# Performance work log

Hardware: AMD Instinct MI355X
Metric: run time of the kernel (lower is better)

The kernel has to match this reference:

```python
import jax, jax.numpy as jnp
import numpy as np

UNITS = 4096                                # number of heap nodes (power of two)
DEPTH = (UNITS - 1).bit_length() + 1        # 13 heap steps (k = 0..12)
FEATURES = [2, 64, 64, 2]
BATCH = 256


def _build_heap_maps(nodes):
    """For each heap step k, precompute for every output node j the input
    (ancestor) node index it reads from, plus a validity mask. This encodes
    exactly the torch block loop: for level l, input nodes [floor(2^(l-1)), 2^l)
    broadcast (repeat_interleave by heap_factor) into output range
    [out_node0, out_node1), with blocks where out_node1 > nodes skipped."""
    depth = (nodes - 1).bit_length() + 1
    maps = []
    for k in range(depth):
        idx = np.zeros(nodes, np.int32)
        mask = np.zeros(nodes, np.bool_)
        for l in range(depth):
            in0 = 0 if l == 0 else 2 ** (l - 1)
            if in0 == 0:  # root block (node 0)
                hf = 1 if k == 0 else 2 ** (k - 1)      # ceil(2^(k-1))
                out0 = 0 if k == 0 else 2 ** (k - 1)    # floor(2^(k-1))
                out1 = out0 + hf
            else:
                hf = 2 ** k
                out0 = in0 * hf
                out1 = (2 ** l) * hf
            if out1 <= nodes:
                js = np.arange(out0, out1)
                idx[js] = in0 + (js - out0) // hf
                mask[js] = True
        maps.append((jnp.asarray(idx), jnp.asarray(mask)))
    return maps


MAPS = _build_heap_maps(UNITS)


def heap_linear(x, W, b, minheap):
    # x: [..., nodes, in_f]; W: [K, out_f, in_f]; b: [K, out_f]; K = DEPTH - minheap
    out = jnp.zeros(x.shape[:-1] + (W.shape[1],), jnp.float32)
    for i, k in enumerate(range(minheap, DEPTH)):
        idx, mask = MAPS[k]
        # apply linear_k to every node once, then gather parent -> children
        y = jnp.einsum('...ni,oi->...no', x, W[i]) + b[i]
        out = out + jnp.where(mask[:, None], y[..., idx, :], 0.0)
    return out


def setup_inputs() -> dict:
    key = jax.random.key(0)
    ks = jax.random.split(key, 7)
    f0, f1, f2, f3 = FEATURES

    def w(k, n, o, i):
        return jax.random.normal(k, (n, o, i), jnp.float32) / np.float32(np.sqrt(i))

    return {
        "x": jax.random.normal(ks[0], (BATCH, UNITS, f0), jnp.float32),
        "W1": w(ks[1], DEPTH - 1, f1, f0),   # minheap=1 -> 12 sublayers
        "b1": jax.random.normal(ks[2], (DEPTH - 1, f1), jnp.float32) * 0.01,
        "W2": w(ks[3], DEPTH, f2, f1),       # minheap=0 -> 13 sublayers
        "b2": jax.random.normal(ks[4], (DEPTH, f2), jnp.float32) * 0.01,
        "W3": w(ks[5], DEPTH, f3, f2),
        "b3": jax.random.normal(ks[6], (DEPTH, f3), jnp.float32) * 0.01,
    }


def reference(x, W1, b1, W2, b2, W3, b3):
    h = heap_linear(x, W1, b1, minheap=1)
    h = jax.nn.relu(h)
    h = heap_linear(h, W2, b2, minheap=0)
    h = jax.nn.relu(h)
    logits = heap_linear(h, W3, b3, minheap=0)
    return logits
```

## Files before the change

kernel.cpp:

```cpp
#include <hip/hip_runtime.h>

#define UNITS 4096
#define DEPTH 13
#define BATCH 256

typedef __attribute__((ext_vector_type(8))) short s16x8;
typedef __attribute__((ext_vector_type(4))) float f32x4;
typedef __attribute__((ext_vector_type(4))) int   i32x4;

__device__ __forceinline__ unsigned short f2bf(float f){
  unsigned u = __builtin_bit_cast(unsigned, f);
  u += 0x7FFFu + ((u >> 16) & 1u);
  return (unsigned short)(u >> 16);
}
__device__ __forceinline__ int levelof(int j){ return j ? (32 - __clz(j)) : 0; }

struct FragA { s16x8 v[2][2]; };
struct FragB { s16x8 v[2][4]; };

__device__ __forceinline__ void load_afrag(FragA& f, const unsigned short* __restrict__ Hq,
                                           int rowbase, int l15, int kg){
  #pragma unroll
  for (int kk = 0; kk < 2; ++kk)
    #pragma unroll
    for (int m = 0; m < 2; ++m)
      f.v[kk][m] = *(const s16x8*)(Hq + ((size_t)((kk*4 + kg)*256 + rowbase + m*16 + l15))*8);
}
__device__ __forceinline__ void load_bfrag(FragB& f, const unsigned short* __restrict__ Wf,
                                           int lane){
  #pragma unroll
  for (int kk = 0; kk < 2; ++kk)
    #pragma unroll
    for (int n = 0; n < 4; ++n)
      f.v[kk][n] = *(const s16x8*)(Wf + ((size_t)((kk*4 + n)*64 + lane))*8);
}
__device__ __forceinline__ void mstep(f32x4 acc[2][4], const FragA& A, const FragB& B){
  #pragma unroll
  for (int kk = 0; kk < 2; ++kk)
    #pragma unroll
    for (int m = 0; m < 2; ++m)
      #pragma unroll
      for (int n = 0; n < 4; ++n)
        acc[m][n] = __builtin_amdgcn_mfma_f32_16x16x32_bf16(A.v[kk][m], B.v[kk][n], acc[m][n], 0, 0, 0);
}
__device__ __forceinline__ void negA(FragA& A){
  const i32x4 sgn = {(int)0x80008000, (int)0x80008000, (int)0x80008000, (int)0x80008000};
  #pragma unroll
  for (int kk = 0; kk < 2; ++kk)
    #pragma unroll
    for (int m = 0; m < 2; ++m){
      i32x4 t = __builtin_bit_cast(i32x4, A.v[kk][m]);
      t ^= sgn;
      A.v[kk][m] = __builtin_bit_cast(s16x8, t);
    }
}

__device__ __forceinline__ float rowsum16(float s){
  int v, u;
  v = __builtin_bit_cast(int, s);
  u = __builtin_amdgcn_update_dpp(v, v, 0xB1, 0xF, 0xF, false);
  s += __builtin_bit_cast(float, u);
  v = __builtin_bit_cast(int, s);
  u = __builtin_amdgcn_update_dpp(v, v, 0x4E, 0xF, 0xF, false);
  s += __builtin_bit_cast(float, u);
  v = __builtin_bit_cast(int, s);
  u = __builtin_amdgcn_update_dpp(v, v, 0x141, 0xF, 0xF, false);
  s += __builtin_bit_cast(float, u);
  v = __builtin_bit_cast(int, s);
  u = __builtin_amdgcn_update_dpp(v, v, 0x140, 0xF, 0xF, false);
  s += __builtin_bit_cast(float, u);
  return s;
}

__device__ __forceinline__ void epilogue(const f32x4 acc[2][4], int p, int lp,
    const float cbv[4], const float* w3s,
    float* __restrict__ y3, int rowbase, int l15, int kg){
  int tmax = 11 - lp;
  for (int tt = 0; tt <= tmax; ++tt){
    float w30[4], w31[4];
    #pragma unroll
    for (int n = 0; n < 4; ++n){
      w30[n] = w3s[(tt*2 + 0)*64 + n*16 + l15];
      w31[n] = w3s[(tt*2 + 1)*64 + n*16 + l15];
    }
    int off = 4096 - (4096 >> tt);
    #pragma unroll
    for (int m = 0; m < 2; ++m)
      #pragma unroll
      for (int reg = 0; reg < 4; ++reg){
        float s0 = 0.f, s1 = 0.f;
        #pragma unroll
        for (int n = 0; n < 4; ++n){
          float hv = fmaxf(acc[m][n][reg] + cbv[n], 0.f);
          s0 = fmaf(w30[n], hv, s0);
          s1 = fmaf(w31[n], hv, s1);
        }
        s0 = rowsum16(s0);
        s1 = rowsum16(s1);
        if (l15 == 0){
          int b = rowbase + m*16 + kg*4 + reg;
          float2 v; v.x = s0; v.y = s1;
          *(float2*)(y3 + ((size_t)(off + p)*256 + b)*2) = v;
        }
      }
  }
}

__global__ __launch_bounds__(256) void k_prep(const float* __restrict__ W2,
    const float* __restrict__ W1, const float* __restrict__ W3,
    const float* __restrict__ b1, const float* __restrict__ b2, const float* __restrict__ b3,
    unsigned short* __restrict__ W2f, unsigned short* __restrict__ W1f,
    float* __restrict__ cb1, float* __restrict__ cb2, float* __restrict__ cb3,
    float* __restrict__ w3h20){
  int blk = blockIdx.x, t = threadIdx.x;
  if (blk < 26){
    int u = blk*256 + t;
    int lane = u & 63, c = (u >> 6) & 7, k = u >> 9;
    int n = c & 3, kk = c >> 2, l15 = lane & 15, kg = lane >> 4;
    s16x8 rr;
    #pragma unroll
    for (int e = 0; e < 8; ++e)
      rr[e] = (short)f2bf(W2[((size_t)(k*64 + n*16 + l15))*64 + kk*32 + kg*8 + e]);
    *(s16x8*)(W2f + (size_t)u*8) = rr;
  } else if (blk == 26){
    int n = t >> 6, lane = t & 63, l15 = lane & 15, kg = lane >> 4;
    int f = n*16 + l15;
    s16x8 r = {0,0,0,0,0,0,0,0};
    #pragma unroll
    for (int j = 0; j < 4; ++j){
      int m = kg*4 + j;
      if (m < DEPTH-1){
        r[2*j]   = (short)f2bf(W1[(m*64 + f)*2]);
        r[2*j+1] = (short)f2bf(W1[(m*64 + f)*2 + 1]);
      }
    }
    *(s16x8*)(W1f + (size_t)t*8) = r;
  } else {
    if (t < 64){
      float r = 0.f;
      cb1[t] = 0.f;
      for (int m = 1; m < DEPTH; ++m){ r += b1[(m-1)*64 + t]; cb1[m*64 + t] = r; }
      float r2 = 0.f;
      for (int m = 0; m < DEPTH; ++m){ r2 += b2[m*64 + t]; cb2[m*64 + t] = r2; }
    } else if (t < 66){
      int o = t - 64;
      float r = 0.f;
      for (int m = 0; m < DEPTH; ++m){ r += b3[m*2 + o]; cb3[m*2 + o] = r; }
    } else if (t >= 128 && t < 128 + DEPTH*2){
      int q = t - 128, tt = q >> 1, o = q & 1;
      float s = 0.f;
      for (int f = 0; f < 64; ++f)
        s = fmaf(W3[(tt*2 + o)*64 + f], fmaxf(b2[f], 0.f), s);
      w3h20[tt*2 + o] = s;
    }
  }
}

__global__ __launch_bounds__(256) void k_xpose(const float* __restrict__ x,
                                               float* __restrict__ xT){
  __shared__ float2 tile[64][65];
  int jb = (blockIdx.x & 63) * 64;
  int bb = (blockIdx.x >> 6) * 64;
  int t = threadIdx.x;
  #pragma unroll
  for (int i = 0; i < 16; ++i){
    int idx = i*256 + t;
    int jj = idx & 63, b = idx >> 6;
    tile[jj][b] = *(const float2*)(x + (((size_t)(bb + b))*UNITS + jb + jj)*2);
  }
  __syncthreads();
  #pragma unroll
  for (int i = 0; i < 16; ++i){
    int idx = i*256 + t;
    int b = idx & 63, jj = idx >> 6;
    *(float2*)(xT + (((size_t)(jb + jj))*BATCH + bb + b)*2) = tile[jj][b];
  }
}

__global__ __launch_bounds__(256) void k_GH(const float* __restrict__ xT,
    const unsigned short* __restrict__ W1f, const float* __restrict__ cb1,
    unsigned short* __restrict__ H){
  __shared__ unsigned short tile[BATCH*64];
  int p = blockIdx.x;
  int lvl = levelof(p);
  int t = threadIdx.x, wid = t >> 6, lane = t & 63, l15 = lane & 15, kg = lane >> 4;

  s16x8 af[4];
  #pragma unroll
  for (int m = 0; m < 4; ++m){
    int b = wid*64 + m*16 + l15;
    s16x8 r = {0,0,0,0,0,0,0,0};
    #pragma unroll
    for (int j = 0; j < 4; ++j){
      int mm = kg*4 + j;
      if (mm <= lvl){
        float2 xv = *(const float2*)(xT + ((size_t)(p >> mm)*BATCH + b)*2);
        r[2*j]   = (short)f2bf(xv.x);
        r[2*j+1] = (short)f2bf(xv.y);
      }
    }
    af[m] = r;
  }
  f32x4 acc[4][4];
  #pragma unroll
  for (int m = 0; m < 4; ++m)
    #pragma unroll
    for (int n = 0; n < 4; ++n) acc[m][n] = (f32x4){0.f,0.f,0.f,0.f};
  #pragma unroll
  for (int n = 0; n < 4; ++n){
    s16x8 bf = *(const s16x8*)(W1f + ((size_t)n*64 + lane)*8);
    #pragma unroll
    for (int m = 0; m < 4; ++m)
      acc[m][n] = __builtin_amdgcn_mfma_f32_16x16x32_bf16(af[m], bf, acc[m][n], 0, 0, 0);
  }
  int lvl1 = lvl + 1;
  float cbv[4];
  #pragma unroll
  for (int n = 0; n < 4; ++n) cbv[n] = cb1[lvl1*64 + n*16 + l15];
  #pragma unroll
  for (int m = 0; m < 4; ++m)
    #pragma unroll
    for (int n = 0; n < 4; ++n)
      #pragma unroll
      for (int i = 0; i < 4; ++i){
        int row = wid*64 + m*16 + kg*4 + i;
        int col = n*16 + l15;
        float v = fmaxf(acc[m][n][i] + cbv[n], 0.f);
        *(unsigned short*)((char*)tile + ((row*128 + col*2) ^ ((row & 7) << 4))) = f2bf(v);
      }
  __syncthreads();
  #pragma unroll
  for (int i = 0; i < 8; ++i){
    s16x8 v = *(const s16x8*)((const char*)tile + ((t*128 + i*16) ^ ((t & 7) << 4)));
    *(s16x8*)(H + (size_t)p*16384 + ((size_t)i*256 + t)*8) = v;
  }
}

#define CHB(slot, kk) if ((kk) <= L) load_bfrag(b##slot, W2f + (size_t)(kk)*4096, lane);
#define CHA(slot, ss) if ((ss)+2 <= L) load_afrag(a##slot, H + ((size_t)(q >> (ss)))*16384, rowbase, l15, kg);
#define CHM(as, bs, ss) if ((ss)+2 <= L) mstep(acc, a##as, b##bs);

__global__ __launch_bounds__(256) void k_F7(const unsigned short* __restrict__ H,
    const unsigned short* __restrict__ W2f, const float* __restrict__ cb2,
    const float* __restrict__ W3, float* __restrict__ y3){
  __shared__ float w3s[26*64];
  int bid = blockIdx.x;
  int sg  = bid >> 9;
  int r   = bid & 511;
  int q   = (r & 7)*64 + (r >> 3);
  int t = threadIdx.x, wid = t >> 6, lane = t & 63, l15 = lane & 15, kg = lane >> 4;
  int rowbase = sg*128 + wid*32;

  #pragma unroll
  for (int i = 0; i < 2; ++i){
    int idx = i*256 + t;
    if (idx < 416) ((float4*)w3s)[idx] = ((const float4*)W3)[idx];
  }
  __syncthreads();

  f32x4 acc[2][4];
  #pragma unroll
  for (int m = 0; m < 2; ++m)
    #pragma unroll
    for (int n = 0; n < 4; ++n) acc[m][n] = (f32x4){0.f,0.f,0.f,0.f};

  if (q == 0){
    FragA A; FragB B;
    for (int p = 0; p < 4; ++p){
      int lp = levelof(p);
      float cbv[4];
      #pragma unroll
      for (int n = 0; n < 4; ++n) cbv[n] = cb2[(lp+1)*64 + n*16 + l15];
      #pragma unroll
      for (int m = 0; m < 2; ++m)
        #pragma unroll
        for (int n = 0; n < 4; ++n) acc[m][n] = (f32x4){0.f,0.f,0.f,0.f};
      for (int k = 0; k <= lp; ++k){
        load_bfrag(B, W2f + (size_t)k*4096, lane);
        load_afrag(A, H + (size_t)(p >> k)*16384, rowbase, l15, kg);
        mstep(acc, A, B);
      }
      epilogue(acc, p, lp, cbv, w3s, y3, rowbase, l15, kg);
    }
    return;
  }

  const int L = levelof(q) + 2;
  float cbv[4];
  #pragma unroll
  for (int n = 0; n < 4; ++n) cbv[n] = cb2[(L+1)*64 + n*16 + l15];

  FragA a0, a1, a2; FragB b0, b1;

  CHB(0,2) CHB(1,3)
  CHA(0,0) CHA(1,1) CHA(2,2)
  CHM(0,0,0) CHB(0,4)  CHA(0,3)
  CHM(1,1,1) CHB(1,5)  CHA(1,4)
  CHM(2,0,2) CHB(0,6)  CHA(2,5)
  CHM(0,1,3) CHB(1,7)  CHA(0,6)
  CHM(1,0,4) CHB(0,8)  CHA(1,7)
  CHM(2,1,5) CHB(1,9)  CHA(2,8)
  CHM(0,0,6) CHB(0,10) CHA(0,9)
  CHM(1,1,7) CHB(1,11)
  load_afrag(a1, H + (size_t)(2*q)*16384, rowbase, l15, kg);
  CHM(2,0,8)
  load_bfrag(b0, W2f + 4096, lane);
  load_afrag(a2, H + (size_t)(4*q)*16384, rowbase, l15, kg);
  CHM(0,1,9)
  load_bfrag(b1, W2f, lane);
  load_afrag(a0, H + (size_t)(4*q + 1)*16384, rowbase, l15, kg);

  mstep(acc, a1, b0);
  mstep(acc, a2, b1);
  epilogue(acc, 4*q, L, cbv, w3s, y3, rowbase, l15, kg);
  negA(a2); mstep(acc, a2, b1);
  load_afrag(a2, H + (size_t)(2*q + 1)*16384, rowbase, l15, kg);
  mstep(acc, a0, b1);
  epilogue(acc, 4*q + 1, L, cbv, w3s, y3, rowbase, l15, kg);
  negA(a0); mstep(acc, a0, b1);
  load_afrag(a0, H + (size_t)(4*q + 2)*16384, rowbase, l15, kg);
  negA(a1); mstep(acc, a1, b0);
  load_afrag(a1, H + (size_t)(4*q + 3)*16384, rowbase, l15, kg);
  mstep(acc, a2, b0);
  mstep(acc, a0, b1);
  epilogue(acc, 4*q + 2, L, cbv, w3s, y3, rowbase, l15, kg);
  negA(a0); mstep(acc, a0, b1);
  mstep(acc, a1, b1);
  epilogue(acc, 4*q + 3, L, cbv, w3s, y3, rowbase, l15, kg);
}

__global__ __launch_bounds__(256) void k_scatter(const float* __restrict__ y3,
    const float* __restrict__ cb3, const float* __restrict__ w3h20,
    float* __restrict__ out){
  int i = blockIdx.x;
  int b = threadIdx.x;
  float4 o[4];
  #pragma unroll
  for (int c = 0; c < 4; ++c){
    int p = i*4 + c;
    int lp = levelof(p);
    float s0 = cb3[(lp+1)*2]     + w3h20[(lp+1)*2];
    float s1 = cb3[(lp+1)*2 + 1] + w3h20[(lp+1)*2 + 1];
    for (int k = 0; k <= lp; ++k){
      int pi = (4096 - (4096 >> k)) + (p >> k);
      float2 v = *(const float2*)(y3 + ((size_t)pi*256 + b)*2);
      s0 += v.x; s1 += v.y;
    }
    if (p == 0){
      o[c].x = cb3[0] + w3h20[0];
      o[c].y = cb3[1] + w3h20[1];
      o[c].z = s0; o[c].w = s1;
    } else {
      o[c].x = s0; o[c].y = s1; o[c].z = s0; o[c].w = s1;
    }
  }
  float4* dst = (float4*)(out + (size_t)b*8192 + (size_t)i*16);
  #pragma unroll
  for (int c = 0; c < 4; ++c) dst[c] = o[c];
}

extern "C" void kernel_launch(void* const* d_in, const int* in_sizes, int n_in,
                              void* d_out, int out_size, void* d_ws, size_t ws_size,
                              hipStream_t stream){
  const float* x  = (const float*)d_in[0];
  const float* W1 = (const float*)d_in[1];
  const float* b1 = (const float*)d_in[2];
  const float* W2 = (const float*)d_in[3];
  const float* b2 = (const float*)d_in[4];
  const float* W3 = (const float*)d_in[5];
  const float* b3 = (const float*)d_in[6];
  float* out = (float*)d_out;
  char* ws = (char*)d_ws;

  unsigned short* W2f   = (unsigned short*)(ws + 0);
  unsigned short* W1f   = (unsigned short*)(ws + 106496);
  float* cb1   = (float*)(ws + 110592);
  float* cb2   = (float*)(ws + 113920);
  float* cb3   = (float*)(ws + 117248);
  float* w3h20 = (float*)(ws + 117376);
  float* xT    = (float*)(ws + 117504);
  unsigned short* H = (unsigned short*)(ws + 8506112);
  float* y3    = (float*)(ws + 75614976);

  hipLaunchKernelGGL(k_prep,    dim3(28),   dim3(256), 0, stream, W2, W1, W3, b1, b2, b3, W2f, W1f, cb1, cb2, cb3, w3h20);
  hipLaunchKernelGGL(k_xpose,   dim3(256),  dim3(256), 0, stream, x, xT);
  hipLaunchKernelGGL(k_GH,      dim3(2048), dim3(256), 0, stream, xT, W1f, cb1, H);
  hipLaunchKernelGGL(k_F7,      dim3(1024), dim3(256), 0, stream, H, W2f, cb2, W3, y3);
  hipLaunchKernelGGL(k_scatter, dim3(512),  dim3(256), 0, stream, y3, cb3, w3h20, out);
}
```

Baseline: 139.5 us.

## Halve per-wave M tile in heap layer-2 kernel, double grid, reverse block order

Each wave in the fused layer-2/3 kernel now computes 16 batch rows instead of 32, which halves the accumulator and A-fragment registers. The grid doubles to 2048 blocks with a 64-row slice per block. Launch bounds now request 3 blocks per SM, and the block-to-node mapping is reversed so the deepest, most expensive nodes are scheduled first. The intent is more occupancy and better load balance, at the cost of reloading each B (weight) fragment twice as often per batch row.

```diff
diff --git a/kernel.cpp b/kernel.cpp
--- a/kernel.cpp
+++ b/kernel.cpp
@@ -15,16 +15,14 @@
 }
 __device__ __forceinline__ int levelof(int j){ return j ? (32 - __clz(j)) : 0; }
 
-struct FragA { s16x8 v[2][2]; };
+struct FragA { s16x8 v[2]; };
 struct FragB { s16x8 v[2][4]; };
 
 __device__ __forceinline__ void load_afrag(FragA& f, const unsigned short* __restrict__ Hq,
                                            int rowbase, int l15, int kg){
   #pragma unroll
   for (int kk = 0; kk < 2; ++kk)
-    #pragma unroll
-    for (int m = 0; m < 2; ++m)
-      f.v[kk][m] = *(const s16x8*)(Hq + ((size_t)((kk*4 + kg)*256 + rowbase + m*16 + l15))*8);
+    f.v[kk] = *(const s16x8*)(Hq + ((size_t)((kk*4 + kg)*256 + rowbase + l15))*8);
 }
 __device__ __forceinline__ void load_bfrag(FragB& f, const unsigned short* __restrict__ Wf,
                                            int lane){
@@ -34,25 +32,21 @@
     for (int n = 0; n < 4; ++n)
       f.v[kk][n] = *(const s16x8*)(Wf + ((size_t)((kk*4 + n)*64 + lane))*8);
 }
-__device__ __forceinline__ void mstep(f32x4 acc[2][4], const FragA& A, const FragB& B){
+__device__ __forceinline__ void mstep(f32x4 acc[4], const FragA& A, const FragB& B){
   #pragma unroll
   for (int kk = 0; kk < 2; ++kk)
     #pragma unroll
-    for (int m = 0; m < 2; ++m)
-      #pragma unroll
-      for (int n = 0; n < 4; ++n)
-        acc[m][n] = __builtin_amdgcn_mfma_f32_16x16x32_bf16(A.v[kk][m], B.v[kk][n], acc[m][n], 0, 0, 0);
+    for (int n = 0; n < 4; ++n)
+      acc[n] = __builtin_amdgcn_mfma_f32_16x16x32_bf16(A.v[kk], B.v[kk][n], acc[n], 0, 0, 0);
 }
 __device__ __forceinline__ void negA(FragA& A){
   const i32x4 sgn = {(int)0x80008000, (int)0x80008000, (int)0x80008000, (int)0x80008000};
   #pragma unroll
-  for (int kk = 0; kk < 2; ++kk)
-    #pragma unroll
-    for (int m = 0; m < 2; ++m){
-      i32x4 t = __builtin_bit_cast(i32x4, A.v[kk][m]);
-      t ^= sgn;
-      A.v[kk][m] = __builtin_bit_cast(s16x8, t);
-    }
+  for (int kk = 0; kk < 2; ++kk){
+    i32x4 t = __builtin_bit_cast(i32x4, A.v[kk]);
+    t ^= sgn;
+    A.v[kk] = __builtin_bit_cast(s16x8, t);
+  }
 }
 
 __device__ __forceinline__ float rowsum16(float s){
@@ -72,7 +66,7 @@
   return s;
 }
 
-__device__ __forceinline__ void epilogue(const f32x4 acc[2][4], int p, int lp,
+__device__ __forceinline__ void epilogue(const f32x4 acc[4], int p, int lp,
     const float cbv[4], const float* w3s,
     float* __restrict__ y3, int rowbase, int l15, int kg){
   int tmax = 11 - lp;
@@ -85,24 +79,22 @@
     }
     int off = 4096 - (4096 >> tt);
     #pragma unroll
-    for (int m = 0; m < 2; ++m)
+    for (int reg = 0; reg < 4; ++reg){
+      float s0 = 0.f, s1 = 0.f;
       #pragma unroll
-      for (int reg = 0; reg < 4; ++reg){
-        float s0 = 0.f, s1 = 0.f;
-        #pragma unroll
-        for (int n = 0; n < 4; ++n){
-          float hv = fmaxf(acc[m][n][reg] + cbv[n], 0.f);
-          s0 = fmaf(w30[n], hv, s0);
-          s1 = fmaf(w31[n], hv, s1);
-        }
-        s0 = rowsum16(s0);
-        s1 = rowsum16(s1);
-        if (l15 == 0){
-          int b = rowbase + m*16 + kg*4 + reg;
-          float2 v; v.x = s0; v.y = s1;
-          *(float2*)(y3 + ((size_t)(off + p)*256 + b)*2) = v;
-        }
-      }
+      for (int n = 0; n < 4; ++n){
+        float hv = fmaxf(acc[n][reg] + cbv[n], 0.f);
+        s0 = fmaf(w30[n], hv, s0);
+        s1 = fmaf(w31[n], hv, s1);
+      }
+      s0 = rowsum16(s0);
+      s1 = rowsum16(s1);
+      if (l15 == 0){
+        int b = rowbase + kg*4 + reg;
+        float2 v; v.x = s0; v.y = s1;
+        *(float2*)(y3 + ((size_t)(off + p)*256 + b)*2) = v;
+      }
+    }
   }
 }
 
@@ -240,16 +232,16 @@
 #define CHA(slot, ss) if ((ss)+2 <= L) load_afrag(a##slot, H + ((size_t)(q >> (ss)))*16384, rowbase, l15, kg);
 #define CHM(as, bs, ss) if ((ss)+2 <= L) mstep(acc, a##as, b##bs);
 
-__global__ __launch_bounds__(256) void k_F7(const unsigned short* __restrict__ H,
+__global__ __launch_bounds__(256, 3) void k_F9(const unsigned short* __restrict__ H,
     const unsigned short* __restrict__ W2f, const float* __restrict__ cb2,
     const float* __restrict__ W3, float* __restrict__ y3){
   __shared__ float w3s[26*64];
   int bid = blockIdx.x;
-  int sg  = bid >> 9;
+  int slice = bid >> 9;
   int r   = bid & 511;
-  int q   = (r & 7)*64 + (r >> 3);
+  int q   = 511 - ((r & 7)*64 + (r >> 3));
   int t = threadIdx.x, wid = t >> 6, lane = t & 63, l15 = lane & 15, kg = lane >> 4;
-  int rowbase = sg*128 + wid*32;
+  int rowbase = slice*64 + wid*16;
 
   #pragma unroll
   for (int i = 0; i < 2; ++i){
@@ -258,11 +250,9 @@
   }
   __syncthreads();
 
-  f32x4 acc[2][4];
-  #pragma unroll
-  for (int m = 0; m < 2; ++m)
-    #pragma unroll
-    for (int n = 0; n < 4; ++n) acc[m][n] = (f32x4){0.f,0.f,0.f,0.f};
+  f32x4 acc[4];
+  #pragma unroll
+  for (int n = 0; n < 4; ++n) acc[n] = (f32x4){0.f, 0.f, 0.f, 0.f};
 
   if (q == 0){
     FragA A; FragB B;
@@ -272,9 +262,7 @@
       #pragma unroll
       for (int n = 0; n < 4; ++n) cbv[n] = cb2[(lp+1)*64 + n*16 + l15];
       #pragma unroll
-      for (int m = 0; m < 2; ++m)
-        #pragma unroll
-        for (int n = 0; n < 4; ++n) acc[m][n] = (f32x4){0.f,0.f,0.f,0.f};
+      for (int n = 0; n < 4; ++n) acc[n] = (f32x4){0.f, 0.f, 0.f, 0.f};
       for (int k = 0; k <= lp; ++k){
         load_bfrag(B, W2f + (size_t)k*4096, lane);
         load_afrag(A, H + (size_t)(p >> k)*16384, rowbase, l15, kg);
@@ -385,6 +373,6 @@
   hipLaunchKernelGGL(k_prep,    dim3(28),   dim3(256), 0, stream, W2, W1, W3, b1, b2, b3, W2f, W1f, cb1, cb2, cb3, w3h20);
   hipLaunchKernelGGL(k_xpose,   dim3(256),  dim3(256), 0, stream, x, xT);
   hipLaunchKernelGGL(k_GH,      dim3(2048), dim3(256), 0, stream, xT, W1f, cb1, H);
-  hipLaunchKernelGGL(k_F7,      dim3(1024), dim3(256), 0, stream, H, W2f, cb2, W3, y3);
+  hipLaunchKernelGGL(k_F9,      dim3(2048), dim3(256), 0, stream, H, W2f, cb2, W3, y3);
   hipLaunchKernelGGL(k_scatter, dim3(512),  dim3(256), 0, stream, y3, cb3, w3h20, out);
 }
```

Result: faster. 121.1 us (-13.2%).
